# Kernel optimization log

Hardware: AMD Instinct MI355X
Metric: run time of the kernel (lower is better)

## Reference

```python
import math
import jax, jax.numpy as jnp
import numpy as np

B, T, S, H, L, NH = 2, 512, 2048, 768, 32, 12
INTERMED = 4 * H


def _make_pe(max_len, hidden):
    position = np.arange(max_len)[:, None].astype(np.float32)
    div_term = np.exp(np.arange(0, hidden, 2).astype(np.float32) * (-math.log(10000.0) / hidden))
    pe = np.zeros((max_len, hidden), dtype=np.float32)
    pe[:, 0::2] = np.sin(position * div_term)
    pe[:, 1::2] = np.cos(position * div_term)
    return jnp.asarray(pe)


def setup_inputs() -> dict:
    key = jax.random.key(0)
    ks = jax.random.split(key, 10)
    token_reps = jax.random.normal(ks[0], (B, T, H), dtype=jnp.float32)
    starts = jax.random.randint(ks[1], (B, S), 0, T - L)
    lens = jax.random.randint(ks[2], (B, S), 1, L + 1)
    span_ids = jnp.stack([starts, starts + lens], axis=-1)  # (B,S,2)
    span_masks = jax.random.uniform(ks[3], (B, S)) > 0.2
    pe = _make_pe(T, H)
    dummy_query = jax.random.normal(ks[4], (H,), dtype=jnp.float32) * 0.02
    in_proj_w = jax.random.normal(ks[5], (3 * H, H), dtype=jnp.float32) * 0.02
    in_proj_b = jnp.zeros((3 * H,), jnp.float32)
    out_proj_w = jax.random.normal(ks[6], (H, H), dtype=jnp.float32) * 0.02
    out_proj_b = jnp.zeros((H,), jnp.float32)
    norm_g = jnp.ones((H,), jnp.float32)
    norm_b = jnp.zeros((H,), jnp.float32)
    ffn_w1 = jax.random.normal(ks[7], (INTERMED, H), dtype=jnp.float32) * (math.sqrt(2.0 / H))
    ffn_b1 = jnp.zeros((INTERMED,), jnp.float32)
    ffn_w2 = jax.random.normal(ks[8], (H, INTERMED), dtype=jnp.float32) * (math.sqrt(2.0 / INTERMED))
    ffn_b2 = jnp.zeros((H,), jnp.float32)
    return dict(token_reps=token_reps, span_ids=span_ids, span_masks=span_masks,
                pooling=0, pe=pe, dummy_query=dummy_query,
                in_proj_w=in_proj_w, in_proj_b=in_proj_b,
                out_proj_w=out_proj_w, out_proj_b=out_proj_b,
                norm_g=norm_g, norm_b=norm_b,
                ffn_w1=ffn_w1, ffn_b1=ffn_b1, ffn_w2=ffn_w2, ffn_b2=ffn_b2)


def _layernorm(x, g, b, eps=1e-5):
    mu = jnp.mean(x, axis=-1, keepdims=True)
    var = jnp.mean(jnp.square(x - mu), axis=-1, keepdims=True)
    return (x - mu) * jax.lax.rsqrt(var + eps) * g + b


def reference(token_reps, span_ids, span_masks, pooling, pe, dummy_query,
              in_proj_w, in_proj_b, out_proj_w, out_proj_b,
              norm_g, norm_b, ffn_w1, ffn_b1, ffn_w2, ffn_b2):
    b, t, h = token_reps.shape
    s = span_ids.shape[1]
    hd = h // NH
    # positional encoding over the sequence (dropout=0 / eval mode)
    x = token_reps + pe[:t]
    # ragged -> padded gather of span tokens
    starts = span_ids[..., 0]
    lens = (span_ids[..., 1] - starts) * span_masks.astype(span_ids.dtype)  # (B,S)
    ar = jnp.arange(L)
    pos = starts[..., None] + ar                     # (B,S,L)
    valid = ar[None, None, :] < lens[..., None]      # (B,S,L) True = real token
    idx = jnp.clip(pos, 0, t - 1)
    gathered = jax.vmap(lambda xb, ib: xb[ib])(x, idx)   # (B,S,L,H)
    gathered = gathered * valid[..., None]
    # guard fully-masked rows (masked-out / zero-len spans): keep one key valid,
    # output is zeroed at the end anyway (matches torch span_reps[~mask]=0)
    any_v = jnp.any(valid, axis=-1)
    valid = valid.at[..., 0].set(valid[..., 0] | ~any_v)
    # single-query multi-head attention (torch nn.MultiheadAttention math)
    Wq, Wk, Wv = jnp.split(in_proj_w, 3, axis=0)
    bq, bk, bv = jnp.split(in_proj_b, 3, axis=0)
    q = (dummy_query @ Wq.T + bq).reshape(NH, hd)                  # (NH,hd)
    k = (gathered @ Wk.T + bk).reshape(b, s, L, NH, hd)
    v = (gathered @ Wv.T + bv).reshape(b, s, L, NH, hd)
    scores = jnp.einsum('nd,bslnd->bsnl', q, k) / math.sqrt(hd)    # (B,S,NH,L)
    scores = jnp.where(valid[:, :, None, :], scores, -jnp.inf)
    attn = jax.nn.softmax(scores, axis=-1)
    ctx = jnp.einsum('bsnl,bslnd->bsnd', attn, v).reshape(b, s, h)
    attn_out = ctx @ out_proj_w.T + out_proj_b
    # residual + LayerNorm, FFN, residual + same LayerNorm
    x1 = _layernorm(attn_out + dummy_query, norm_g, norm_b)
    ffn = jax.nn.relu(x1 @ ffn_w1.T + ffn_b1) @ ffn_w2.T + ffn_b2
    out = _layernorm(ffn + x1, norm_g, norm_b)
    out = out * span_masks[..., None]
    return out
```

## Files before the change

kernel.cpp:

```cpp
#include <hip/hip_runtime.h>
#include <math.h>

static constexpr int B_  = 2;
static constexpr int T_  = 512;
static constexpr int S_  = 2048;
static constexpr int H_  = 768;
static constexpr int L_  = 32;
static constexpr int NH_ = 12;
static constexpr int HD_ = 64;
static constexpr int IM_ = 3072;

typedef __bf16 bf16x8 __attribute__((ext_vector_type(8)));
typedef float  f32x4  __attribute__((ext_vector_type(4)));

__device__ __forceinline__ float bf2f(unsigned short u) {
    return __uint_as_float(((unsigned)u) << 16);
}
__device__ __forceinline__ unsigned short f2bf(float f) {
    unsigned u = __float_as_uint(f);
    u += 0x7fffu + ((u >> 16) & 1u);
    return (unsigned short)(u >> 16);
}
__device__ __forceinline__ void gl_lds16(const void* g, void* l) {
    __builtin_amdgcn_global_load_lds((const __attribute__((address_space(1))) void*)g,
                                     (__attribute__((address_space(3))) void*)l, 16, 0, 0);
}

__global__ void k_q(const float* __restrict__ dq, const float* __restrict__ w,
                    const float* __restrict__ b, float* __restrict__ q,
                    const int* __restrict__ raw, int* __restrict__ mout) {
    int wv = threadIdx.x >> 6, lane = threadIdx.x & 63;
    int i = blockIdx.x * 4 + wv;
    const float* row = w + (size_t)i * H_;
    float acc = 0.f;
#pragma unroll
    for (int k = 0; k < 12; ++k) acc += dq[lane + 64 * k] * row[lane + 64 * k];
    for (int m = 32; m; m >>= 1) acc += __shfl_xor(acc, m, 64);
    if (lane == 0) q[i] = acc + b[i];
    if (blockIdx.x == 0) {
        __shared__ int bad;
        if (threadIdx.x == 0) bad = 0;
        __syncthreads();
        for (int t = threadIdx.x; t < 1024; t += 256) {
            int v = raw[t];
            if (v != 0 && v != 1) bad = 1;
        }
        __syncthreads();
        int byte_layout = bad;
        const unsigned char* rb = (const unsigned char*)raw;
        for (int t = threadIdx.x; t < B_ * S_; t += 256)
            mout[t] = byte_layout ? (int)rb[t] : raw[t];
    }
}

static constexpr int CWB = 2880;
__global__ void k_castw(const float* __restrict__ s0, const float* __restrict__ s1,
                        const float* __restrict__ s2, const float* __restrict__ s3,
                        unsigned short* __restrict__ d0, unsigned short* __restrict__ d1,
                        unsigned short* __restrict__ d2, unsigned short* __restrict__ d3,
                        const float* __restrict__ q, const float* __restrict__ wk,
                        float* __restrict__ wq) {
    if (blockIdx.x >= CWB) {
        int i = (blockIdx.x - CWB) * 256 + threadIdx.x;
        int n = i / H_, hh = i % H_;
        float acc = 0.f;
        for (int d = 0; d < HD_; ++d)
            acc += q[n * HD_ + d] * wk[(size_t)(H_ + n * HD_ + d) * H_ + hh];
        wq[i] = acc;
        return;
    }
    const long n0 = (long)H_ * H_, n2 = (long)IM_ * H_;
    long gid = (long)(blockIdx.x * 256 + threadIdx.x) * 8;
    const float* s; unsigned short* d; long off;
    if (gid < n0)                { s = s0; d = d0; off = gid; }
    else if (gid < 2 * n0)       { s = s1; d = d1; off = gid - n0; }
    else if (gid < 2 * n0 + n2)  { s = s2; d = d2; off = gid - 2 * n0; }
    else                         { s = s3; d = d3; off = gid - 2 * n0 - n2; }
    float4 f0 = *(const float4*)(s + off);
    float4 f1 = *(const float4*)(s + off + 4);
    uint4 o;
    o.x = (unsigned)f2bf(f0.x) | ((unsigned)f2bf(f0.y) << 16);
    o.y = (unsigned)f2bf(f0.z) | ((unsigned)f2bf(f0.w) << 16);
    o.z = (unsigned)f2bf(f1.x) | ((unsigned)f2bf(f1.y) << 16);
    o.w = (unsigned)f2bf(f1.z) | ((unsigned)f2bf(f1.w) << 16);
    *(uint4*)(d + off) = o;
}

__global__ void k_xstok(const float* __restrict__ tr, const float* __restrict__ pe,
                        const float* __restrict__ wq,
                        unsigned short* __restrict__ xbf, float* __restrict__ stok) {
    __shared__ float sx[H_];
    int bt = blockIdx.x, tid = threadIdx.x;
    const float* trow = tr + (size_t)bt * H_;
    const float* prow = pe + (size_t)(bt % T_) * H_;
    if (tid < 192) {
        int h0 = tid * 4;
        float4 a = *(const float4*)(trow + h0);
        float4 p = *(const float4*)(prow + h0);
        float v0 = a.x + p.x, v1 = a.y + p.y, v2 = a.z + p.z, v3 = a.w + p.w;
        sx[h0] = v0; sx[h0 + 1] = v1; sx[h0 + 2] = v2; sx[h0 + 3] = v3;
        uint2 o;
        o.x = (unsigned)f2bf(v0) | ((unsigned)f2bf(v1) << 16);
        o.y = (unsigned)f2bf(v2) | ((unsigned)f2bf(v3) << 16);
        *(uint2*)(xbf + (size_t)bt * H_ + h0) = o;
    }
    __syncthreads();
    int lane = tid & 63, w = tid >> 6;
    float xv[12];
#pragma unroll
    for (int k = 0; k < 12; ++k) xv[k] = sx[lane + 64 * k];
#pragma unroll
    for (int hh = 0; hh < 3; ++hh) {
        int n = w * 3 + hh;
        const float* wr = wq + (size_t)n * H_;
        float acc = 0.f;
#pragma unroll
        for (int k = 0; k < 12; ++k) acc += xv[k] * wr[lane + 64 * k];
        for (int m = 32; m; m >>= 1) acc += __shfl_xor(acc, m, 64);
        if (lane == 0) stok[bt * NH_ + n] = acc;
    }
}

__global__ void k_castv4(const unsigned short* __restrict__ p, size_t pstr,
                         unsigned short* __restrict__ dst, int n) {
    int i = (blockIdx.x * 256 + threadIdx.x) * 8;
    if (i >= n) return;
    float a[8] = {};
#pragma unroll
    for (int z = 0; z < 4; ++z) {
        uint4 u = *(const uint4*)(p + z * pstr + i);
        a[0] += bf2f((unsigned short)(u.x & 0xffff));
        a[1] += bf2f((unsigned short)(u.x >> 16));
        a[2] += bf2f((unsigned short)(u.y & 0xffff));
        a[3] += bf2f((unsigned short)(u.y >> 16));
        a[4] += bf2f((unsigned short)(u.z & 0xffff));
        a[5] += bf2f((unsigned short)(u.z >> 16));
        a[6] += bf2f((unsigned short)(u.w & 0xffff));
        a[7] += bf2f((unsigned short)(u.w >> 16));
    }
    uint4 o;
    o.x = (unsigned)f2bf(a[0]) | ((unsigned)f2bf(a[1]) << 16);
    o.y = (unsigned)f2bf(a[2]) | ((unsigned)f2bf(a[3]) << 16);
    o.z = (unsigned)f2bf(a[4]) | ((unsigned)f2bf(a[5]) << 16);
    o.w = (unsigned)f2bf(a[6]) | ((unsigned)f2bf(a[7]) << 16);
    *(uint4*)(dst + i) = o;
}

#define STG3(b_, k0e_) do {                                                   \
    unsigned short* _la = AsB + (b_) * 4096 + wid * 1024;                     \
    unsigned short* _lb = BsB + (b_) * 4096 + wid * 1024;                     \
    gl_lds16(agp + (k0e_), _la);                                              \
    gl_lds16(agp + (size_t)16 * K + (k0e_), _la + 512);                       \
    gl_lds16(bgp + (k0e_), _lb);                                              \
    gl_lds16(bgp + (size_t)16 * K + (k0e_), _lb + 512);                       \
} while (0)

template <bool RELU, bool SPLIT>
__device__ __forceinline__
void gemm_d3_body(const unsigned short* __restrict__ A, const unsigned short* __restrict__ W,
                  const float* __restrict__ bias, unsigned short* __restrict__ Cout,
                  int M, int N, int K, int kLen, int TX, int SP) {
    __shared__ unsigned short As[3][4096];
    __shared__ unsigned short Bs[3][4096];
    unsigned short* const AsB = &As[0][0];
    unsigned short* const BsB = &Bs[0][0];
    const int qx = blockIdx.x & 7, t = blockIdx.x >> 3;
    const int gi = t / TX, x = t - gi * TX;
    const int g = gi * 8 + qx;
    int y, z;
    if (SPLIT) { y = g / SP; z = g - y * SP; } else { y = g; z = 0; }
    const int bm = y * 128, bn = x * 128;
    const int kOff = z * kLen;

    const int tid = threadIdx.x, lane = tid & 63, wid = tid >> 6;
    const int wm = (wid >> 1) * 64, wn = (wid & 1) * 64;
    const int r16 = lane >> 2, c4 = lane & 3;
    const int swc = (c4 ^ ((r16 >> 1) & 3)) * 8;
    const unsigned short* agp = A + (size_t)(bm + wid * 32 + r16) * K + kOff + swc;
    const unsigned short* bgp = W + (size_t)(bn + wid * 32 + r16) * K + kOff + swc;

    f32x4 acc[4][4];
#pragma unroll
    for (int i = 0; i < 4; ++i)
#pragma unroll
        for (int j = 0; j < 4; ++j) acc[i][j] = f32x4{0.f, 0.f, 0.f, 0.f};

    const int mrow = lane & 15;
    const int q4 = lane >> 4;
    const int sw = (q4 ^ ((mrow >> 1) & 3)) * 8;
    const int NIT = kLen >> 5;

    STG3(0, 0);
    STG3(1, 1 << 5);
    int c0 = 0, c1 = 1, c2 = 2;
    for (int it = 0; it < NIT; ++it) {
        int nk = it + 2; if (nk > NIT - 1) nk = NIT - 1;
        STG3(c2, nk << 5);
        asm volatile("s_waitcnt vmcnt(8)" ::: "memory");
        __builtin_amdgcn_s_barrier();
        __builtin_amdgcn_sched_barrier(0);
        const unsigned short* Ac = AsB + c0 * 4096;
        const unsigned short* Bc = BsB + c0 * 4096;
        bf16x8 af[4], bfr[4];
#pragma unroll
        for (int i = 0; i < 4; ++i)
            af[i] = *(const bf16x8*)(Ac + (wm + i * 16 + mrow) * 32 + sw);
#pragma unroll
        for (int j = 0; j < 4; ++j)
            bfr[j] = *(const bf16x8*)(Bc + (wn + j * 16 + mrow) * 32 + sw);
        asm volatile("s_waitcnt lgkmcnt(0)" ::: "memory");
        __builtin_amdgcn_sched_barrier(0);
#pragma unroll
        for (int i = 0; i < 4; ++i)
#pragma unroll
            for (int j = 0; j < 4; ++j)
                acc[i][j] = __builtin_amdgcn_mfma_f32_16x16x32_bf16(af[i], bfr[j], acc[i][j], 0, 0, 0);
        __builtin_amdgcn_s_barrier();
        __builtin_amdgcn_sched_barrier(0);
        int tmp = c0; c0 = c1; c1 = c2; c2 = tmp;
    }
    asm volatile("s_waitcnt vmcnt(0)" ::: "memory");

    const bool addb = !SPLIT || z == 0;
    unsigned short* outp = SPLIT ? Cout + (size_t)z * M * N : Cout;
    const int lr = (lane >> 4) * 4, lc = lane & 15;
#pragma unroll
    for (int j = 0; j < 4; ++j) {
        int col = bn + wn + j * 16 + lc;
        float bv = addb ? bias[col] : 0.f;
#pragma unroll
        for (int i = 0; i < 4; ++i) {
            int row0 = bm + wm + i * 16 + lr;
#pragma unroll
            for (int r = 0; r < 4; ++r) {
                float v = acc[i][j][r] + bv;
                if (RELU) v = fmaxf(v, 0.f);
                outp[(size_t)(row0 + r) * N + col] = f2bf(v);
            }
        }
    }
}

__global__ __launch_bounds__(256)
void g3_vtok(const unsigned short* A, const unsigned short* W, const float* bias,
             unsigned short* Cout, int M, int N, int K, int kLen, int TX, int SP) {
    gemm_d3_body<false, true>(A, W, bias, Cout, M, N, K, kLen, TX, SP);
}
__global__ __launch_bounds__(256)
void g3_oproj(const unsigned short* A, const unsigned short* W, const float* bias,
              unsigned short* Cout, int M, int N, int K, int kLen, int TX, int SP) {
    gemm_d3_body<false, true>(A, W, bias, Cout, M, N, K, kLen, TX, SP);
}
__global__ __launch_bounds__(256)
void g3_ffn2(const unsigned short* A, const unsigned short* W, const float* bias,
             unsigned short* Cout, int M, int N, int K, int kLen, int TX, int SP) {
    gemm_d3_body<false, true>(A, W, bias, Cout, M, N, K, kLen, TX, SP);
}

__global__ __launch_bounds__(512)
void g8_ffn1(const unsigned short* __restrict__ A, const unsigned short* __restrict__ W,
             const float* __restrict__ bias, unsigned short* __restrict__ Cout,
             int M, int N, int K, int kLen, int TX) {
    __shared__ unsigned short As[3][8192];
    __shared__ unsigned short Bs[3][4096];
    unsigned short* const AsB = &As[0][0];
    unsigned short* const BsB = &Bs[0][0];
    const int qx = blockIdx.x & 7, t = blockIdx.x >> 3;
    const int gi = t / TX, x = t - gi * TX;
    const int y = gi * 8 + qx;
    const int bm = y * 256, bn = x * 128;

    const int tid = threadIdx.x, lane = tid & 63, wid = tid >> 6;
    const int wm = (wid >> 1) * 64, wn = (wid & 1) * 64;
    const int r16 = lane >> 2, c4 = lane & 3;
    const int swc = (c4 ^ ((r16 >> 1) & 3)) * 8;
    const unsigned short* agp = A + (size_t)(bm + wid * 32 + r16) * K + swc;
    const unsigned short* bgp = W + (size_t)(bn + wid * 16 + r16) * K + swc;

#define STG8(b_, k0e_) do {                                                   \
    unsigned short* _la = AsB + (b_) * 8192 + wid * 1024;                     \
    unsigned short* _lb = BsB + (b_) * 4096 + wid * 512;                      \
    gl_lds16(agp + (k0e_), _la);                                              \
    gl_lds16(agp + (size_t)16 * K + (k0e_), _la + 512);                       \
    gl_lds16(bgp + (k0e_), _lb);                                              \
} while (0)

    f32x4 acc[4][4];
#pragma unroll
    for (int i = 0; i < 4; ++i)
#pragma unroll
        for (int j = 0; j < 4; ++j) acc[i][j] = f32x4{0.f, 0.f, 0.f, 0.f};

    const int mrow = lane & 15;
    const int q4 = lane >> 4;
    const int sw = (q4 ^ ((mrow >> 1) & 3)) * 8;
    const int NIT = kLen >> 5;

    STG8(0, 0);
    STG8(1, 1 << 5);
    int c0 = 0, c1 = 1, c2 = 2;
    for (int it = 0; it < NIT; ++it) {
        int nk = it + 2; if (nk > NIT - 1) nk = NIT - 1;
        STG8(c2, nk << 5);
        asm volatile("s_waitcnt vmcnt(6)" ::: "memory");
        __builtin_amdgcn_s_barrier();
        __builtin_amdgcn_sched_barrier(0);
        const unsigned short* Ac = AsB + c0 * 8192;
        const unsigned short* Bc = BsB + c0 * 4096;
        bf16x8 af[4], bfr[4];
#pragma unroll
        for (int i = 0; i < 4; ++i)
            af[i] = *(const bf16x8*)(Ac + (wm + i * 16 + mrow) * 32 + sw);
#pragma unroll
        for (int j = 0; j < 4; ++j)
            bfr[j] = *(const bf16x8*)(Bc + (wn + j * 16 + mrow) * 32 + sw);
        asm volatile("s_waitcnt lgkmcnt(0)" ::: "memory");
        __builtin_amdgcn_sched_barrier(0);
#pragma unroll
        for (int i = 0; i < 4; ++i)
#pragma unroll
            for (int j = 0; j < 4; ++j)
                acc[i][j] = __builtin_amdgcn_mfma_f32_16x16x32_bf16(af[i], bfr[j], acc[i][j], 0, 0, 0);
        __builtin_amdgcn_s_barrier();
        __builtin_amdgcn_sched_barrier(0);
        int tmp = c0; c0 = c1; c1 = c2; c2 = tmp;
    }
    asm volatile("s_waitcnt vmcnt(0)" ::: "memory");

    const int lr = (lane >> 4) * 4, lc = lane & 15;
#pragma unroll
    for (int j = 0; j < 4; ++j) {
        int col = bn + wn + j * 16 + lc;
        float bv = bias[col];
#pragma unroll
        for (int i = 0; i < 4; ++i) {
            int row0 = bm + wm + i * 16 + lr;
#pragma unroll
            for (int r = 0; r < 4; ++r) {
                float v = fmaxf(acc[i][j][r] + bv, 0.f);
                Cout[(size_t)(row0 + r) * N + col] = f2bf(v);
            }
        }
    }
#undef STG8
}

__global__ void k_attn(const float* __restrict__ stok, const unsigned short* __restrict__ vtok,
                       const int* __restrict__ span_ids, const int* __restrict__ masks,
                       unsigned short* __restrict__ ctx) {
    int r = blockIdx.x, b = r / S_;
    unsigned short* out = ctx + (size_t)r * H_;
    int tid = threadIdx.x;
    __shared__ float w[NH_][L_];
    __shared__ int idxs[L_];
    __shared__ int s_len;
    if (tid == 0) {
        int m = masks[r];
        int st = span_ids[2 * r], en = span_ids[2 * r + 1];
        int len = m ? (en - st) : 0;
        len = len < 0 ? 0 : (len > L_ ? L_ : len);
        s_len = len;
    }
    __syncthreads();
    int len = s_len;
    if (len == 0) {
        for (int h2 = tid; h2 < H_ / 2; h2 += 256) ((unsigned*)out)[h2] = 0u;
        return;
    }
    if (tid < L_) {
        int p = span_ids[2 * r] + tid;
        idxs[tid] = p < 0 ? 0 : (p > T_ - 1 ? T_ - 1 : p);
    }
    __syncthreads();
    for (int i = tid; i < NH_ * L_; i += 256) {
        int n = i / L_, l = i % L_;
        w[n][l] = (l < len) ? stok[(size_t)(b * T_ + idxs[l]) * NH_ + n] * 0.125f : -INFINITY;
    }
    __syncthreads();
    if (tid < NH_) {
        float mx = -INFINITY;
        for (int l = 0; l < len; ++l) mx = fmaxf(mx, w[tid][l]);
        float sum = 0.f;
        for (int l = 0; l < len; ++l) { float e = __expf(w[tid][l] - mx); w[tid][l] = e; sum += e; }
        float inv = 1.f / sum;
        for (int l = 0; l < len; ++l) w[tid][l] *= inv;
    }
    __syncthreads();
    if (tid < 192) {
        int h0 = tid * 4, n = h0 >> 6;
        float a0 = 0.f, a1 = 0.f, a2 = 0.f, a3 = 0.f;
        for (int l = 0; l < len; ++l) {
            float wl = w[n][l];
            const unsigned short* vr = vtok + (size_t)(b * T_ + idxs[l]) * H_ + h0;
            uint2 u = *(const uint2*)vr;
            a0 += wl * bf2f((unsigned short)(u.x & 0xffff));
            a1 += wl * bf2f((unsigned short)(u.x >> 16));
            a2 += wl * bf2f((unsigned short)(u.y & 0xffff));
            a3 += wl * bf2f((unsigned short)(u.y >> 16));
        }
        uint2 o;
        o.x = (unsigned)f2bf(a0) | ((unsigned)f2bf(a1) << 16);
        o.y = (unsigned)f2bf(a2) | ((unsigned)f2bf(a3) << 16);
        *(uint2*)(out + h0) = o;
    }
}

template <bool RESROW, bool MASKOUT, int ZN>
__global__ void k_ln(const unsigned short* __restrict__ parts, size_t pstr,
                     const float* __restrict__ resf, const unsigned short* __restrict__ resb,
                     const float* __restrict__ g, const float* __restrict__ bt,
                     float* __restrict__ outf, unsigned short* __restrict__ outb,
                     const int* __restrict__ masks) {
    int r = blockIdx.x;
    int tid = threadIdx.x;
    float v[3];
    float lsum = 0.f;
#pragma unroll
    for (int i = 0; i < 3; ++i) {
        int h = tid + 256 * i;
        float s = RESROW ? bf2f(resb[(size_t)r * H_ + h]) : resf[h];
#pragma unroll
        for (int z = 0; z < ZN; ++z)
            s += bf2f(parts[z * pstr + (size_t)r * H_ + h]);
        v[i] = s;
        lsum += s;
    }
    __shared__ float sh[256];
    sh[tid] = lsum;
    __syncthreads();
    for (int st = 128; st > 0; st >>= 1) {
        if (tid < st) sh[tid] += sh[tid + st];
        __syncthreads();
    }
    float mean = sh[0] * (1.f / H_);
    __syncthreads();
    float lvar = 0.f;
#pragma unroll
    for (int i = 0; i < 3; ++i) { float d = v[i] - mean; lvar += d * d; }
    sh[tid] = lvar;
    __syncthreads();
    for (int st = 128; st > 0; st >>= 1) {
        if (tid < st) sh[tid] += sh[tid + st];
        __syncthreads();
    }
    float var = sh[0] * (1.f / H_);
    float scale = rsqrtf(var + 1e-5f);
    float mfac = 1.f;
    if (MASKOUT) mfac = masks[r] ? 1.f : 0.f;
#pragma unroll
    for (int i = 0; i < 3; ++i) {
        int h = tid + 256 * i;
        float o = ((v[i] - mean) * scale * g[h] + bt[h]) * mfac;
        if (MASKOUT) outf[(size_t)r * H_ + h] = o;
        else         outb[(size_t)r * H_ + h] = f2bf(o);
    }
}

extern "C" void kernel_launch(void* const* d_in, const int* in_sizes, int n_in,
                              void* d_out, int out_size, void* d_ws, size_t ws_size,
                              hipStream_t stream) {
    const float* token_reps = (const float*)d_in[0];
    const int*   span_ids   = (const int*)d_in[1];
    const int*   masks_raw  = (const int*)d_in[2];
    const float* pe   = (const float*)d_in[4];
    const float* dq   = (const float*)d_in[5];
    const float* in_w = (const float*)d_in[6];
    const float* in_b = (const float*)d_in[7];
    const float* ow   = (const float*)d_in[8];
    const float* ob   = (const float*)d_in[9];
    const float* g    = (const float*)d_in[10];
    const float* bt   = (const float*)d_in[11];
    const float* w1   = (const float*)d_in[12];
    const float* b1   = (const float*)d_in[13];
    const float* w2   = (const float*)d_in[14];
    const float* b2   = (const float*)d_in[15];

    const int BS = B_ * S_;
    const int BT = B_ * T_;

    float* fws   = (float*)d_ws;
    float* stok  = fws;
    float* qv    = stok + BT * NH_;
    float* wqeff = qv + H_;
    unsigned short* us = (unsigned short*)(wqeff + NH_ * H_);
    unsigned short* pbuf = us;
    unsigned short* xbf  = pbuf + (size_t)4 * BS * H_;
    unsigned short* vtok = xbf + (size_t)BT * H_;
    unsigned short* ctx  = vtok + (size_t)BT * H_;
    unsigned short* x1bf = ctx + (size_t)BS * H_;
    unsigned short* f1   = x1bf + (size_t)BS * H_;
    unsigned short* wvb  = f1 + (size_t)BS * IM_;
    unsigned short* owb  = wvb + H_ * H_;
    unsigned short* w1b  = owb + H_ * H_;
    unsigned short* w2b  = w1b + IM_ * H_;
    int* maskn = (int*)(w2b + H_ * IM_);

    k_q<<<H_ / 4, 256, 0, stream>>>(dq, in_w, in_b, qv, masks_raw, maskn);
    k_castw<<<CWB + 36, 256, 0, stream>>>(
        in_w + (size_t)2 * H_ * H_, ow, w1, w2, wvb, owb, w1b, w2b,
        qv, in_w, wqeff);
    k_xstok<<<BT, 256, 0, stream>>>(token_reps, pe, wqeff, xbf, stok);
    g3_vtok<<<192, 256, 0, stream>>>(
        xbf, wvb, in_b + 2 * H_, pbuf, BT, H_, H_, H_ / 4, 6, 4);
    k_castv4<<<(BT * H_ / 8 + 255) / 256, 256, 0, stream>>>(
        pbuf, (size_t)BT * H_, vtok, BT * H_);
    k_attn<<<BS, 256, 0, stream>>>(stok, vtok, span_ids, maskn, ctx);
    g3_oproj<<<384, 256, 0, stream>>>(
        ctx, owb, ob, pbuf, BS, H_, H_, H_ / 2, 6, 2);
    k_ln<false, false, 2><<<BS, 256, 0, stream>>>(
        pbuf, (size_t)BS * H_, dq, nullptr, g, bt, nullptr, x1bf, nullptr);
    g8_ffn1<<<384, 512, 0, stream>>>(
        x1bf, w1b, b1, f1, BS, IM_, H_, H_, 24);
    g3_ffn2<<<384, 256, 0, stream>>>(
        f1, w2b, b2, pbuf, BS, H_, IM_, IM_ / 2, 6, 2);
    k_ln<true, true, 2><<<BS, 256, 0, stream>>>(
        pbuf, (size_t)BS * H_, nullptr, x1bf, g, bt, (float*)d_out, nullptr, maskn);
}
```

Before: 242.7 us.

## Replace oproj/FFN GEMMs with 128x96-tile double-buffered kernel and split-K 4

Introduces a new GEMM body using 128x96 output tiles with 4 waves, double-buffered LDS staging and optional split-K. The out-projection, FFN1 and FFN2 GEMMs now use it with 1024 blocks each, and oproj/ffn2 go from split-K 2 to 4 with the LayerNorm kernels summing 4 partials. The goal is better CU occupancy and load balance on the many-CU GPU. The cost is smaller tiles with lower data reuse, shallower pipelining than the old 3-stage FFN1 kernel, and more partial-sum traffic.

```diff
diff --git a/kernel.cpp b/kernel.cpp
--- a/kernel.cpp
+++ b/kernel.cpp
@@ -246,103 +246,117 @@
              unsigned short* Cout, int M, int N, int K, int kLen, int TX, int SP) {
     gemm_d3_body<false, true>(A, W, bias, Cout, M, N, K, kLen, TX, SP);
 }
-__global__ __launch_bounds__(256)
-void g3_oproj(const unsigned short* A, const unsigned short* W, const float* bias,
-              unsigned short* Cout, int M, int N, int K, int kLen, int TX, int SP) {
-    gemm_d3_body<false, true>(A, W, bias, Cout, M, N, K, kLen, TX, SP);
-}
-__global__ __launch_bounds__(256)
-void g3_ffn2(const unsigned short* A, const unsigned short* W, const float* bias,
-             unsigned short* Cout, int M, int N, int K, int kLen, int TX, int SP) {
-    gemm_d3_body<false, true>(A, W, bias, Cout, M, N, K, kLen, TX, SP);
-}
-
-__global__ __launch_bounds__(512)
-void g8_ffn1(const unsigned short* __restrict__ A, const unsigned short* __restrict__ W,
-             const float* __restrict__ bias, unsigned short* __restrict__ Cout,
-             int M, int N, int K, int kLen, int TX) {
-    __shared__ unsigned short As[3][8192];
-    __shared__ unsigned short Bs[3][4096];
+
+template <bool RELU, bool SPLIT>
+__device__ __forceinline__
+void gemm_n96_body(const unsigned short* __restrict__ A, const unsigned short* __restrict__ W,
+                   const float* __restrict__ bias, unsigned short* __restrict__ Cout,
+                   int M, int N, int K, int kLen, int TX, int SP) {
+    __shared__ unsigned short As[2][4096];
+    __shared__ unsigned short Bs[2][3072];
     unsigned short* const AsB = &As[0][0];
     unsigned short* const BsB = &Bs[0][0];
     const int qx = blockIdx.x & 7, t = blockIdx.x >> 3;
     const int gi = t / TX, x = t - gi * TX;
-    const int y = gi * 8 + qx;
-    const int bm = y * 256, bn = x * 128;
+    const int g = gi * 8 + qx;
+    int y, z;
+    if (SPLIT) { y = g / SP; z = g - y * SP; } else { y = g; z = 0; }
+    const int bm = y * 128, bn = x * 96;
+    const int kOff = z * kLen;
 
     const int tid = threadIdx.x, lane = tid & 63, wid = tid >> 6;
-    const int wm = (wid >> 1) * 64, wn = (wid & 1) * 64;
+    const int wm = (wid >> 1) * 64, wn = (wid & 1) * 48;
     const int r16 = lane >> 2, c4 = lane & 3;
     const int swc = (c4 ^ ((r16 >> 1) & 3)) * 8;
-    const unsigned short* agp = A + (size_t)(bm + wid * 32 + r16) * K + swc;
-    const unsigned short* bgp = W + (size_t)(bn + wid * 16 + r16) * K + swc;
-
-#define STG8(b_, k0e_) do {                                                   \
-    unsigned short* _la = AsB + (b_) * 8192 + wid * 1024;                     \
-    unsigned short* _lb = BsB + (b_) * 4096 + wid * 512;                      \
+    const unsigned short* agp = A + (size_t)(bm + wid * 32 + r16) * K + kOff + swc;
+    const unsigned short* bgp  = W + (size_t)(bn + wid * 16 + r16) * K + kOff + swc;
+    const unsigned short* bgp2 = W + (size_t)(bn + 64 + wid * 16 + r16) * K + kOff + swc;
+
+#define STG96(b_, k0e_) do {                                                  \
+    unsigned short* _la = AsB + (b_) * 4096 + wid * 1024;                     \
     gl_lds16(agp + (k0e_), _la);                                              \
     gl_lds16(agp + (size_t)16 * K + (k0e_), _la + 512);                       \
-    gl_lds16(bgp + (k0e_), _lb);                                              \
+    gl_lds16(bgp + (k0e_), BsB + (b_) * 3072 + wid * 512);                    \
+    if (wid < 2)                                                              \
+        gl_lds16(bgp2 + (k0e_), BsB + (b_) * 3072 + (4 + wid) * 512);         \
 } while (0)
 
-    f32x4 acc[4][4];
+    f32x4 acc[4][3];
 #pragma unroll
     for (int i = 0; i < 4; ++i)
 #pragma unroll
-        for (int j = 0; j < 4; ++j) acc[i][j] = f32x4{0.f, 0.f, 0.f, 0.f};
+        for (int j = 0; j < 3; ++j) acc[i][j] = f32x4{0.f, 0.f, 0.f, 0.f};
 
     const int mrow = lane & 15;
     const int q4 = lane >> 4;
     const int sw = (q4 ^ ((mrow >> 1) & 3)) * 8;
     const int NIT = kLen >> 5;
 
-    STG8(0, 0);
-    STG8(1, 1 << 5);
-    int c0 = 0, c1 = 1, c2 = 2;
+    STG96(0, 0);
     for (int it = 0; it < NIT; ++it) {
-        int nk = it + 2; if (nk > NIT - 1) nk = NIT - 1;
-        STG8(c2, nk << 5);
-        asm volatile("s_waitcnt vmcnt(6)" ::: "memory");
+        const int cur = it & 1;
+        int nk = it + 1; if (nk > NIT - 1) nk = NIT - 1;
+        STG96(cur ^ 1, nk << 5);
+        if (wid < 2) { asm volatile("s_waitcnt vmcnt(4)" ::: "memory"); }
+        else         { asm volatile("s_waitcnt vmcnt(3)" ::: "memory"); }
         __builtin_amdgcn_s_barrier();
         __builtin_amdgcn_sched_barrier(0);
-        const unsigned short* Ac = AsB + c0 * 8192;
-        const unsigned short* Bc = BsB + c0 * 4096;
-        bf16x8 af[4], bfr[4];
+        const unsigned short* Ac = AsB + cur * 4096;
+        const unsigned short* Bc = BsB + cur * 3072;
+        bf16x8 af[4], bfr[3];
 #pragma unroll
         for (int i = 0; i < 4; ++i)
             af[i] = *(const bf16x8*)(Ac + (wm + i * 16 + mrow) * 32 + sw);
 #pragma unroll
-        for (int j = 0; j < 4; ++j)
+        for (int j = 0; j < 3; ++j)
             bfr[j] = *(const bf16x8*)(Bc + (wn + j * 16 + mrow) * 32 + sw);
         asm volatile("s_waitcnt lgkmcnt(0)" ::: "memory");
         __builtin_amdgcn_sched_barrier(0);
 #pragma unroll
         for (int i = 0; i < 4; ++i)
 #pragma unroll
-            for (int j = 0; j < 4; ++j)
+            for (int j = 0; j < 3; ++j)
                 acc[i][j] = __builtin_amdgcn_mfma_f32_16x16x32_bf16(af[i], bfr[j], acc[i][j], 0, 0, 0);
         __builtin_amdgcn_s_barrier();
         __builtin_amdgcn_sched_barrier(0);
-        int tmp = c0; c0 = c1; c1 = c2; c2 = tmp;
     }
     asm volatile("s_waitcnt vmcnt(0)" ::: "memory");
 
+    const bool addb = !SPLIT || z == 0;
+    unsigned short* outp = SPLIT ? Cout + (size_t)z * M * N : Cout;
     const int lr = (lane >> 4) * 4, lc = lane & 15;
 #pragma unroll
-    for (int j = 0; j < 4; ++j) {
+    for (int j = 0; j < 3; ++j) {
         int col = bn + wn + j * 16 + lc;
-        float bv = bias[col];
+        float bv = addb ? bias[col] : 0.f;
 #pragma unroll
         for (int i = 0; i < 4; ++i) {
             int row0 = bm + wm + i * 16 + lr;
 #pragma unroll
             for (int r = 0; r < 4; ++r) {
-                float v = fmaxf(acc[i][j][r] + bv, 0.f);
-                Cout[(size_t)(row0 + r) * N + col] = f2bf(v);
+                float v = acc[i][j][r] + bv;
+                if (RELU) v = fmaxf(v, 0.f);
+                outp[(size_t)(row0 + r) * N + col] = f2bf(v);
             }
         }
     }
-#undef STG8
+#undef STG96
+}
+
+__global__ __launch_bounds__(256)
+void g96_oproj(const unsigned short* A, const unsigned short* W, const float* bias,
+               unsigned short* Cout, int M, int N, int K, int kLen, int TX, int SP) {
+    gemm_n96_body<false, true>(A, W, bias, Cout, M, N, K, kLen, TX, SP);
+}
+__global__ __launch_bounds__(256)
+void g96_ffn1(const unsigned short* A, const unsigned short* W, const float* bias,
+              unsigned short* Cout, int M, int N, int K, int kLen, int TX, int SP) {
+    gemm_n96_body<true, false>(A, W, bias, Cout, M, N, K, kLen, TX, SP);
+}
+__global__ __launch_bounds__(256)
+void g96_ffn2(const unsigned short* A, const unsigned short* W, const float* bias,
+              unsigned short* Cout, int M, int N, int K, int kLen, int TX, int SP) {
+    gemm_n96_body<false, true>(A, W, bias, Cout, M, N, K, kLen, TX, SP);
 }
 
 __global__ void k_attn(const float* __restrict__ stok, const unsigned short* __restrict__ vtok,
@@ -505,14 +519,14 @@
     k_castv4<<<(BT * H_ / 8 + 255) / 256, 256, 0, stream>>>(
         pbuf, (size_t)BT * H_, vtok, BT * H_);
     k_attn<<<BS, 256, 0, stream>>>(stok, vtok, span_ids, maskn, ctx);
-    g3_oproj<<<384, 256, 0, stream>>>(
-        ctx, owb, ob, pbuf, BS, H_, H_, H_ / 2, 6, 2);
-    k_ln<false, false, 2><<<BS, 256, 0, stream>>>(
+    g96_oproj<<<1024, 256, 0, stream>>>(
+        ctx, owb, ob, pbuf, BS, H_, H_, H_ / 4, 8, 4);
+    k_ln<false, false, 4><<<BS, 256, 0, stream>>>(
         pbuf, (size_t)BS * H_, dq, nullptr, g, bt, nullptr, x1bf, nullptr);
-    g8_ffn1<<<384, 512, 0, stream>>>(
-        x1bf, w1b, b1, f1, BS, IM_, H_, H_, 24);
-    g3_ffn2<<<384, 256, 0, stream>>>(
-        f1, w2b, b2, pbuf, BS, H_, IM_, IM_ / 2, 6, 2);
-    k_ln<true, true, 2><<<BS, 256, 0, stream>>>(
+    g96_ffn1<<<1024, 256, 0, stream>>>(
+        x1bf, w1b, b1, f1, BS, IM_, H_, H_, 32, 1);
+    g96_ffn2<<<1024, 256, 0, stream>>>(
+        f1, w2b, b2, pbuf, BS, H_, IM_, IM_ / 4, 8, 4);
+    k_ln<true, true, 4><<<BS, 256, 0, stream>>>(
         pbuf, (size_t)BS * H_, nullptr, x1bf, g, bt, (float*)d_out, nullptr, maskn);
 }
```

Result: no change. 247.3 us (+1.9%).
